# Performance work log

Hardware: AMD Instinct MI355X
Metric: run time of the kernel (lower is better)

Reference implementation:

```python
import jax, jax.numpy as jnp
import numpy as np
from jax import lax

# ---- ConvBlock config (matches init_kwargs) ----
IN_CH, OUT_CH, K, MB = 64, 128, 3, 8
P = OUT_CH // MB            # 16 block-rows
Q = (IN_CH * K * K) // MB   # 72 block-cols (64*9=576, divisible by 8)
BN_EPS = 1e-5
ACT_THRES = 6.0


def setup_inputs() -> dict:
    key = jax.random.key(0)
    k1, k2, k3, k4 = jax.random.split(key, 4)
    x = jax.random.normal(k1, (32, IN_CH, 56, 56), dtype=jnp.float32)
    # block-decomposed MZI weight: [p, q, mb, mb]
    fan_in = IN_CH * K * K
    w_blocks = jax.random.normal(k2, (P, Q, MB, MB), dtype=jnp.float32) * (1.0 / np.sqrt(fan_in))
    gamma = jax.random.uniform(k3, (OUT_CH,), dtype=jnp.float32, minval=0.5, maxval=1.5)
    beta = jax.random.normal(k4, (OUT_CH,), dtype=jnp.float32) * 0.1
    return {"x": x, "w_blocks": w_blocks, "gamma": gamma, "beta": beta}


def _assemble_weight(w_blocks):
    # [p, q, mb, mb] -> dense [p*mb, q*mb] -> crop -> [O, I, K, K]
    p, q, mb, _ = w_blocks.shape
    w = jnp.transpose(w_blocks, (0, 2, 1, 3)).reshape(p * mb, q * mb)
    w = w[:OUT_CH, : IN_CH * K * K]
    return w.reshape(OUT_CH, IN_CH, K, K)


def reference(x, w_blocks, gamma, beta):
    # MZIBlockConv2d, weight mode, w_bit=in_bit=16 => quantizers are identity,
    # photodetect=False => plain real-valued conv with block-assembled weight.
    w = _assemble_weight(w_blocks)
    y = lax.conv_general_dilated(
        x, w,
        window_strides=(1, 1),
        padding=((1, 1), (1, 1)),
        dimension_numbers=("NCHW", "OIHW", "NCHW"),
    )
    # BatchNorm2d in training mode: batch statistics over (N, H, W), biased var
    mean = jnp.mean(y, axis=(0, 2, 3))
    var = jnp.var(y, axis=(0, 2, 3))
    inv = gamma / jnp.sqrt(var + BN_EPS)
    y = (y - mean[None, :, None, None]) * inv[None, :, None, None] + beta[None, :, None, None]
    # ReLUN(6): clipped ReLU
    return jnp.clip(y, 0.0, ACT_THRES)
```

## Files before the change

kernel.cpp:

```cpp
#include <hip/hip_runtime.h>

#define NB    32
#define CIN   64
#define COUT  128
#define HH    56
#define WW    56
#define NPIX  (NB*HH*WW)
#define BN_EPSF 1e-5f

typedef __bf16 bf16x8 __attribute__((ext_vector_type(8)));
typedef float  f32x4  __attribute__((ext_vector_type(4)));
typedef unsigned short u16x8 __attribute__((ext_vector_type(8)));

__global__ void zero_sums(float* g) {
    g[threadIdx.x] = 0.0f;
}

__global__ void assemble_w(const float* __restrict__ wb,
                           __bf16* __restrict__ whi, __bf16* __restrict__ wlo) {
    int idx = blockIdx.x * 256 + threadIdx.x;
    if (idx >= 576 * 128) return;
    int col = idx >> 7, oc = idx & 127;
    int p = oc >> 3, i = oc & 7, q = col >> 3, j = col & 7;
    float v = wb[((p * 72 + q) * 8 + i) * 8 + j];
    int ic = col / 9, tap = col % 9;
    int dst = ((tap * 2 + (ic >> 5)) * 128 + oc) * 32 + (ic & 31);
    __bf16 hi = (__bf16)v;
    whi[dst] = hi;
    wlo[dst] = (__bf16)(v - (float)hi);
}

__global__ __launch_bounds__(256, 4) void conv_mfma(
    const float* __restrict__ x, const __bf16* __restrict__ whi,
    const __bf16* __restrict__ wlo, float* __restrict__ y,
    float* __restrict__ gsum, float* __restrict__ gsq)
{
    __shared__ __bf16 xs_hi[160 * 64];
    __shared__ __bf16 xs_lo[160 * 64];

    int b = blockIdx.x;
    int n = b / 28, t = b % 28;
    int h0 = (t / 7) * 14, w0 = (t % 7) * 8;
    int tid  = threadIdx.x;
    int lane = tid & 63, wid = tid >> 6;
    int l15 = lane & 15, l4 = lane >> 4;
    int oc0 = wid * 32;

    const float* xn = x + n * CIN * HH * WW;
    for (int u = tid; u < 1280; u += 256) {
        int c = u / 160, px = u - c * 160;
        int r = px / 10, cc = px - r * 10;
        int gh = h0 - 1 + r, gw = w0 - 1 + cc;
        bool ok = ((unsigned)gh < 56u) & ((unsigned)gw < 56u);
        const float* src = xn + (c * 8) * (HH * WW) + gh * WW + gw;
        bf16x8 hi, lo;
        #pragma unroll
        for (int j = 0; j < 8; ++j) {
            float v = ok ? src[j * HH * WW] : 0.0f;
            __bf16 h = (__bf16)v;
            hi[j] = h;
            lo[j] = (__bf16)(v - (float)h);
        }
        int dst = px * 64 + ((c ^ (px & 7)) * 8);
        *(bf16x8*)&xs_hi[dst] = hi;
        *(bf16x8*)&xs_lo[dst] = lo;
    }
    __syncthreads();

    f32x4 acc[7][2] = {};

    for (int tap = 0; tap < 9; ++tap) {
        int kh = tap / 3, kw = tap - kh * 3;
        #pragma unroll
        for (int half = 0; half < 2; ++half) {
            const __bf16* bh = whi + ((tap * 2 + half) * 128) * 32;
            const __bf16* bl = wlo + ((tap * 2 + half) * 128) * 32;
            bf16x8 bh0 = *(const bf16x8*)&bh[(oc0 +      l15) * 32 + l4 * 8];
            bf16x8 bh1 = *(const bf16x8*)&bh[(oc0 + 16 + l15) * 32 + l4 * 8];
            bf16x8 bl0 = *(const bf16x8*)&bl[(oc0 +      l15) * 32 + l4 * 8];
            bf16x8 bl1 = *(const bf16x8*)&bl[(oc0 + 16 + l15) * 32 + l4 * 8];
            int cbase = half * 4 + l4;

            #pragma unroll
            for (int mt = 0; mt < 7; ++mt) {
                int px = mt * 16 + l15;
                int R  = ((px >> 3) + kh) * 10 + (px & 7) + kw;
                int ae = R * 64 + ((cbase ^ (R & 7)) * 8);
                bf16x8 ah = *(const bf16x8*)&xs_hi[ae];
                bf16x8 al = *(const bf16x8*)&xs_lo[ae];
                acc[mt][0] = __builtin_amdgcn_mfma_f32_16x16x32_bf16(ah, bh0, acc[mt][0], 0, 0, 0);
                acc[mt][1] = __builtin_amdgcn_mfma_f32_16x16x32_bf16(ah, bh1, acc[mt][1], 0, 0, 0);
                acc[mt][0] = __builtin_amdgcn_mfma_f32_16x16x32_bf16(ah, bl0, acc[mt][0], 0, 0, 0);
                acc[mt][1] = __builtin_amdgcn_mfma_f32_16x16x32_bf16(ah, bl1, acc[mt][1], 0, 0, 0);
                acc[mt][0] = __builtin_amdgcn_mfma_f32_16x16x32_bf16(al, bh0, acc[mt][0], 0, 0, 0);
                acc[mt][1] = __builtin_amdgcn_mfma_f32_16x16x32_bf16(al, bh1, acc[mt][1], 0, 0, 0);
            }
        }
    }

    float* yn = y + n * COUT * HH * WW;
    int pyb = l4 >> 1;
    int gwo = w0 + (l4 & 1) * 4;
    #pragma unroll
    for (int mt = 0; mt < 7; ++mt) {
        int gh = h0 + mt * 2 + pyb;
        #pragma unroll
        for (int nt = 0; nt < 2; ++nt) {
            int oc = oc0 + nt * 16 + l15;
            *(float4*)&yn[(oc * HH + gh) * WW + gwo] = *(float4*)&acc[mt][nt];
        }
    }

    float* red = (float*)xs_hi;
    __syncthreads();
    #pragma unroll
    for (int nt = 0; nt < 2; ++nt) {
        float s = 0.0f, sq = 0.0f;
        #pragma unroll
        for (int mt = 0; mt < 7; ++mt)
            #pragma unroll
            for (int r = 0; r < 4; ++r) {
                float v = acc[mt][nt][r];
                s += v; sq += v * v;
            }
        s  += __shfl_xor(s, 16, 64);  s  += __shfl_xor(s, 32, 64);
        sq += __shfl_xor(sq, 16, 64); sq += __shfl_xor(sq, 32, 64);
        if (l4 == 0) {
            int oc = oc0 + nt * 16 + l15;
            red[oc] = s; red[128 + oc] = sq;
        }
    }
    __syncthreads();
    if (tid < 128) {
        atomicAdd(&gsum[tid], red[tid]);
        atomicAdd(&gsq[tid],  red[128 + tid]);
    }
}

__global__ void bn_finalize(const float* __restrict__ gsum, const float* __restrict__ gsq,
                            const float* __restrict__ gamma, const float* __restrict__ beta,
                            float* __restrict__ scale, float* __restrict__ shift)
{
    int c = threadIdx.x;
    float mean = gsum[c] * (1.0f / NPIX);
    float var  = gsq[c]  * (1.0f / NPIX) - mean * mean;
    float inv  = gamma[c] / sqrtf(var + BN_EPSF);
    scale[c] = inv;
    shift[c] = beta[c] - mean * inv;
}

__global__ __launch_bounds__(256) void bn_apply(float* __restrict__ y,
        const float* __restrict__ scale, const float* __restrict__ shift)
{
    const int total4 = NB * COUT * HH * WW / 4;
    int idx = blockIdx.x * blockDim.x + threadIdx.x;
    int stride = gridDim.x * blockDim.x;
    for (int i4 = idx; i4 < total4; i4 += stride) {
        int c = (i4 / 784) & 127;
        float sc = scale[c], sh = shift[c];
        float4 v = ((float4*)y)[i4];
        v.x = fminf(fmaxf(fmaf(v.x, sc, sh), 0.0f), 6.0f);
        v.y = fminf(fmaxf(fmaf(v.y, sc, sh), 0.0f), 6.0f);
        v.z = fminf(fmaxf(fmaf(v.z, sc, sh), 0.0f), 6.0f);
        v.w = fminf(fmaxf(fmaf(v.w, sc, sh), 0.0f), 6.0f);
        ((float4*)y)[i4] = v;
    }
}

extern "C" void kernel_launch(void* const* d_in, const int* in_sizes, int n_in,
                              void* d_out, int out_size, void* d_ws, size_t ws_size,
                              hipStream_t stream) {
    const float* x     = (const float*)d_in[0];
    const float* wb    = (const float*)d_in[1];
    const float* gamma = (const float*)d_in[2];
    const float* beta  = (const float*)d_in[3];
    float* y = (float*)d_out;

    __bf16* whi = (__bf16*)d_ws;
    __bf16* wlo = whi + 73728;
    float* gsum  = (float*)(wlo + 73728);
    float* gsq   = gsum + 128;
    float* scale = gsq + 128;
    float* shift = scale + 128;

    zero_sums<<<1, 256, 0, stream>>>(gsum);
    assemble_w<<<(576 * 128 + 255) / 256, 256, 0, stream>>>(wb, whi, wlo);
    conv_mfma<<<NB * 28, 256, 0, stream>>>(x, whi, wlo, y, gsum, gsq);
    bn_finalize<<<1, COUT, 0, stream>>>(gsum, gsq, gamma, beta, scale, shift);
    bn_apply<<<2048, 256, 0, stream>>>(y, scale, shift);
}
```

Baseline: 163.2 us.

## Drop split-bf16 compensation terms and shrink conv tiles to 8x8 pixels

Removes the hi/lo bf16 split of inputs and weights, so each product takes one MFMA instead of three and only a single bf16 copy is staged in shared memory. The spatial tile shrinks from 14x8 to 8x8 output pixels, giving 49 blocks per image, a smaller LDS footprint, and a higher occupancy target in launch bounds. This cuts MFMA work and LDS traffic but lowers accuracy to plain bf16, which risks exceeding the fp32 reference tolerance. Halo overhead per block also rises with the smaller tiles.

```diff
diff --git a/kernel.cpp b/kernel.cpp
--- a/kernel.cpp
+++ b/kernel.cpp
@@ -10,14 +10,12 @@
 
 typedef __bf16 bf16x8 __attribute__((ext_vector_type(8)));
 typedef float  f32x4  __attribute__((ext_vector_type(4)));
-typedef unsigned short u16x8 __attribute__((ext_vector_type(8)));
 
 __global__ void zero_sums(float* g) {
     g[threadIdx.x] = 0.0f;
 }
 
-__global__ void assemble_w(const float* __restrict__ wb,
-                           __bf16* __restrict__ whi, __bf16* __restrict__ wlo) {
+__global__ void assemble_w(const float* __restrict__ wb, __bf16* __restrict__ whi) {
     int idx = blockIdx.x * 256 + threadIdx.x;
     if (idx >= 576 * 128) return;
     int col = idx >> 7, oc = idx & 127;
@@ -25,76 +23,61 @@
     float v = wb[((p * 72 + q) * 8 + i) * 8 + j];
     int ic = col / 9, tap = col % 9;
     int dst = ((tap * 2 + (ic >> 5)) * 128 + oc) * 32 + (ic & 31);
-    __bf16 hi = (__bf16)v;
-    whi[dst] = hi;
-    wlo[dst] = (__bf16)(v - (float)hi);
+    whi[dst] = (__bf16)v;
 }
 
-__global__ __launch_bounds__(256, 4) void conv_mfma(
+__global__ __launch_bounds__(256, 8) void conv_mfma(
     const float* __restrict__ x, const __bf16* __restrict__ whi,
-    const __bf16* __restrict__ wlo, float* __restrict__ y,
-    float* __restrict__ gsum, float* __restrict__ gsq)
+    float* __restrict__ y, float* __restrict__ gsum, float* __restrict__ gsq)
 {
-    __shared__ __bf16 xs_hi[160 * 64];
-    __shared__ __bf16 xs_lo[160 * 64];
+    __shared__ __bf16 xs[100 * 64];
 
     int b = blockIdx.x;
-    int n = b / 28, t = b % 28;
-    int h0 = (t / 7) * 14, w0 = (t % 7) * 8;
+    int n = b / 49, t = b % 49;
+    int h0 = (t / 7) * 8, w0 = (t % 7) * 8;
     int tid  = threadIdx.x;
     int lane = tid & 63, wid = tid >> 6;
     int l15 = lane & 15, l4 = lane >> 4;
     int oc0 = wid * 32;
 
     const float* xn = x + n * CIN * HH * WW;
-    for (int u = tid; u < 1280; u += 256) {
-        int c = u / 160, px = u - c * 160;
+    for (int u = tid; u < 800; u += 256) {
+        int c = u / 100, px = u - c * 100;
         int r = px / 10, cc = px - r * 10;
         int gh = h0 - 1 + r, gw = w0 - 1 + cc;
         bool ok = ((unsigned)gh < 56u) & ((unsigned)gw < 56u);
         const float* src = xn + (c * 8) * (HH * WW) + gh * WW + gw;
-        bf16x8 hi, lo;
+        bf16x8 hv;
         #pragma unroll
         for (int j = 0; j < 8; ++j) {
             float v = ok ? src[j * HH * WW] : 0.0f;
-            __bf16 h = (__bf16)v;
-            hi[j] = h;
-            lo[j] = (__bf16)(v - (float)h);
+            hv[j] = (__bf16)v;
         }
-        int dst = px * 64 + ((c ^ (px & 7)) * 8);
-        *(bf16x8*)&xs_hi[dst] = hi;
-        *(bf16x8*)&xs_lo[dst] = lo;
+        *(bf16x8*)&xs[px * 64 + ((c ^ (px & 7)) * 8)] = hv;
     }
     __syncthreads();
 
-    f32x4 acc[7][2] = {};
+    f32x4 acc[4][2] = {};
 
-    for (int tap = 0; tap < 9; ++tap) {
-        int kh = tap / 3, kw = tap - kh * 3;
+    int rb0  = (l15 >> 3) * 10 + (l15 & 7);
+    int woff = (oc0 + l15) * 32 + l4 * 8;
+
+    #pragma unroll 2
+    for (int th = 0; th < 18; ++th) {
+        int tap = th >> 1, half = th & 1;
+        int kh = (tap * 11) >> 5;
+        int toff = kh * 10 + (tap - kh * 3);
+        const __bf16* bp = whi + th * 4096;
+        bf16x8 b0 = *(const bf16x8*)&bp[woff];
+        bf16x8 b1 = *(const bf16x8*)&bp[woff + 512];
+        int c0 = half * 4 + l4;
         #pragma unroll
-        for (int half = 0; half < 2; ++half) {
-            const __bf16* bh = whi + ((tap * 2 + half) * 128) * 32;
-            const __bf16* bl = wlo + ((tap * 2 + half) * 128) * 32;
-            bf16x8 bh0 = *(const bf16x8*)&bh[(oc0 +      l15) * 32 + l4 * 8];
-            bf16x8 bh1 = *(const bf16x8*)&bh[(oc0 + 16 + l15) * 32 + l4 * 8];
-            bf16x8 bl0 = *(const bf16x8*)&bl[(oc0 +      l15) * 32 + l4 * 8];
-            bf16x8 bl1 = *(const bf16x8*)&bl[(oc0 + 16 + l15) * 32 + l4 * 8];
-            int cbase = half * 4 + l4;
-
-            #pragma unroll
-            for (int mt = 0; mt < 7; ++mt) {
-                int px = mt * 16 + l15;
-                int R  = ((px >> 3) + kh) * 10 + (px & 7) + kw;
-                int ae = R * 64 + ((cbase ^ (R & 7)) * 8);
-                bf16x8 ah = *(const bf16x8*)&xs_hi[ae];
-                bf16x8 al = *(const bf16x8*)&xs_lo[ae];
-                acc[mt][0] = __builtin_amdgcn_mfma_f32_16x16x32_bf16(ah, bh0, acc[mt][0], 0, 0, 0);
-                acc[mt][1] = __builtin_amdgcn_mfma_f32_16x16x32_bf16(ah, bh1, acc[mt][1], 0, 0, 0);
-                acc[mt][0] = __builtin_amdgcn_mfma_f32_16x16x32_bf16(ah, bl0, acc[mt][0], 0, 0, 0);
-                acc[mt][1] = __builtin_amdgcn_mfma_f32_16x16x32_bf16(ah, bl1, acc[mt][1], 0, 0, 0);
-                acc[mt][0] = __builtin_amdgcn_mfma_f32_16x16x32_bf16(al, bh0, acc[mt][0], 0, 0, 0);
-                acc[mt][1] = __builtin_amdgcn_mfma_f32_16x16x32_bf16(al, bh1, acc[mt][1], 0, 0, 0);
-            }
+        for (int mt = 0; mt < 4; ++mt) {
+            int R  = rb0 + mt * 20 + toff;
+            int ae = R * 64 + ((c0 ^ (R & 7)) * 8);
+            bf16x8 ah = *(const bf16x8*)&xs[ae];
+            acc[mt][0] = __builtin_amdgcn_mfma_f32_16x16x32_bf16(ah, b0, acc[mt][0], 0, 0, 0);
+            acc[mt][1] = __builtin_amdgcn_mfma_f32_16x16x32_bf16(ah, b1, acc[mt][1], 0, 0, 0);
         }
     }
 
@@ -102,7 +85,7 @@
     int pyb = l4 >> 1;
     int gwo = w0 + (l4 & 1) * 4;
     #pragma unroll
-    for (int mt = 0; mt < 7; ++mt) {
+    for (int mt = 0; mt < 4; ++mt) {
         int gh = h0 + mt * 2 + pyb;
         #pragma unroll
         for (int nt = 0; nt < 2; ++nt) {
@@ -111,13 +94,13 @@
         }
     }
 
-    float* red = (float*)xs_hi;
+    float* red = (float*)xs;
     __syncthreads();
     #pragma unroll
     for (int nt = 0; nt < 2; ++nt) {
         float s = 0.0f, sq = 0.0f;
         #pragma unroll
-        for (int mt = 0; mt < 7; ++mt)
+        for (int mt = 0; mt < 4; ++mt)
             #pragma unroll
             for (int r = 0; r < 4; ++r) {
                 float v = acc[mt][nt][r];
@@ -177,15 +160,14 @@
     float* y = (float*)d_out;
 
     __bf16* whi = (__bf16*)d_ws;
-    __bf16* wlo = whi + 73728;
-    float* gsum  = (float*)(wlo + 73728);
+    float* gsum  = (float*)(whi + 73728);
     float* gsq   = gsum + 128;
     float* scale = gsq + 128;
     float* shift = scale + 128;
 
     zero_sums<<<1, 256, 0, stream>>>(gsum);
-    assemble_w<<<(576 * 128 + 255) / 256, 256, 0, stream>>>(wb, whi, wlo);
-    conv_mfma<<<NB * 28, 256, 0, stream>>>(x, whi, wlo, y, gsum, gsq);
+    assemble_w<<<(576 * 128 + 255) / 256, 256, 0, stream>>>(wb, whi);
+    conv_mfma<<<NB * 49, 256, 0, stream>>>(x, whi, y, gsum, gsq);
     bn_finalize<<<1, COUT, 0, stream>>>(gsum, gsq, gamma, beta, scale, shift);
     bn_apply<<<2048, 256, 0, stream>>>(y, scale, shift);
 }
```

Measured after the change: 173.7 us. 1.06x slower.
